# Performance work log

Measured on AMD Instinct MI355X. Metric: run time of the kernel, lower is better.

Reference implementation:

```python
import jax, jax.numpy as jnp
import numpy as np

N_NODES = 50000
N_EDGES = 800000
NFEAT, NHID, NCLASS = 512, 128, 40


def _glorot(key, fan_in, fan_out):
    # mimics the usual GCN uniform init: U(-1/sqrt(fan_out), 1/sqrt(fan_out))
    stdv = 1.0 / np.sqrt(fan_out)
    return jax.random.uniform(key, (fan_in, fan_out), jnp.float32, -stdv, stdv)


def setup_inputs() -> dict:
    key = jax.random.key(0)
    ks = jax.random.split(key, 8)
    x = jax.random.normal(ks[0], (N_NODES, NFEAT), jnp.float32)
    edge_src = jax.random.randint(ks[1], (N_EDGES,), 0, N_NODES)
    edge_dst = jax.random.randint(ks[2], (N_EDGES,), 0, N_NODES)
    edge_weight = jax.random.uniform(ks[3], (N_EDGES,), jnp.float32)
    W1 = _glorot(ks[4], NFEAT, NHID)
    b1 = jnp.zeros((NHID,), jnp.float32)
    W2 = _glorot(ks[5], NHID, NCLASS)
    b2 = jnp.zeros((NCLASS,), jnp.float32)
    return {"x": x, "edge_src": edge_src, "edge_dst": edge_dst,
            "edge_weight": edge_weight, "W1": W1, "b1": b1, "W2": W2, "b2": b2}


def _gcn_layer(x, W, b, edge_src, edge_dst, edge_weight):
    # support = x @ W ; out = spmm(adj, support) + b
    support = x @ W                                   # [N, F_out]
    msgs = support[edge_src] * edge_weight[:, None]   # [E, F_out]
    agg = jax.ops.segment_sum(msgs, edge_dst, num_segments=N_NODES)
    return agg + b


def reference(x, edge_src, edge_dst, edge_weight, W1, b1, W2, b2):
    h = _gcn_layer(x, W1, b1, edge_src, edge_dst, edge_weight)
    h = jax.nn.relu(h)
    # F.dropout(training=False) -> identity in eval mode
    out = _gcn_layer(h, W2, b2, edge_src, edge_dst, edge_weight)
    return out
```

## Files before the change

### kernel.cpp

```cpp
#include <hip/hip_runtime.h>


#define F0 512
#define F1 128
#define F2 40
#define F2P 48

typedef short bf16x8 __attribute__((ext_vector_type(8)));
typedef float f32x4 __attribute__((ext_vector_type(4)));

static __device__ __forceinline__ unsigned short f2b(float f){
    union { float f; unsigned int u; } x; x.f = f;
    unsigned int u = x.u;
    unsigned int r = (u + 0x7fffu + ((u >> 16) & 1u)) >> 16;
    return (unsigned short)r;
}
static __device__ __forceinline__ unsigned short f2b_fast(float f){
    return (unsigned short)((__float_as_uint(f) + 0x8000u) >> 16);
}
static __device__ __forceinline__ unsigned int pack2(float a, float b){
    unsigned int ua = __float_as_uint(a) + 0x8000u;
    unsigned int ub = __float_as_uint(b) + 0x8000u;
    return __builtin_amdgcn_perm(ub, ua, 0x07060302u);
}
static __device__ __forceinline__ bf16x8 pack8(float4 v0, float4 v1){
    union { bf16x8 v; unsigned int d[4]; } r;
    r.d[0] = pack2(v0.x, v0.y);
    r.d[1] = pack2(v0.z, v0.w);
    r.d[2] = pack2(v1.x, v1.y);
    r.d[3] = pack2(v1.z, v1.w);
    return r.v;
}
static __device__ __forceinline__ float b2f(unsigned short h){
    union { unsigned int u; float f; } x; x.u = ((unsigned int)h) << 16; return x.f;
}
static __device__ __forceinline__ unsigned short f2h(float f){
    union { _Float16 h; unsigned short u; } x; x.h = (_Float16)f; return x.u;
}
static __device__ __forceinline__ float h2f(unsigned short u){
    union { unsigned short u; _Float16 h; } x; x.u = u; return (float)x.h;
}

__global__ void prep_w(const float* __restrict__ W1, const float* __restrict__ W2,
                       unsigned short* __restrict__ W1t, unsigned short* __restrict__ W2t,
                       int* __restrict__ cnt8, int n8){
    int idx = blockIdx.x*256 + threadIdx.x;
    if (idx < n8) cnt8[idx] = 0;
    if (idx < F0*F1){
        int k = idx >> 7, n = idx & 127;
        W1t[(size_t)n*F0 + k] = f2b(W1[idx]);
    } else if (idx < F0*F1 + F2P*F1){
        int j = idx - F0*F1;
        int n = j >> 7, k = j & 127;
        float v = (n < F2) ? W2[(size_t)k*F2 + n] : 0.f;
        W2t[j] = f2b(v);
    }
}

__global__ void hist_kernel(const int* __restrict__ dst, int* __restrict__ cnt8,
                            unsigned short* __restrict__ slot, int E){
    int e = blockIdx.x*256 + threadIdx.x;
    if (e < E){
        int d = dst[e];
        int s = e & 7;
        slot[e] = (unsigned short)atomicAdd(&cnt8[d*8 + s], 1);
    }
}

__global__ void scan1_kernel(const int* __restrict__ cnt8, int* __restrict__ offs,
                             unsigned short* __restrict__ lsp, int* __restrict__ bsum, int n){
    __shared__ int sd[256];
    int tid = threadIdx.x;
    int base = blockIdx.x*1024 + tid*4;
    int t[4];
    #pragma unroll
    for (int j=0;j<4;j++){
        int node = base+j;
        int tot = 0;
        if (node < n){
            int4 c0 = *(const int4*)&cnt8[(size_t)node*8];
            int4 c1 = *(const int4*)&cnt8[(size_t)node*8+4];
            unsigned short lp0=0, lp1, lp2, lp3, lp4, lp5, lp6, lp7;
            int run = c0.x; lp1=(unsigned short)run;
            run += c0.y; lp2=(unsigned short)run;
            run += c0.z; lp3=(unsigned short)run;
            run += c0.w; lp4=(unsigned short)run;
            run += c1.x; lp5=(unsigned short)run;
            run += c1.y; lp6=(unsigned short)run;
            run += c1.z; lp7=(unsigned short)run;
            run += c1.w; tot = run;
            ushort4 a, b;
            a.x=lp0; a.y=lp1; a.z=lp2; a.w=lp3;
            b.x=lp4; b.y=lp5; b.z=lp6; b.w=lp7;
            *(ushort4*)&lsp[(size_t)node*8]   = a;
            *(ushort4*)&lsp[(size_t)node*8+4] = b;
        }
        t[j] = tot;
    }
    int v1=t[0], v2=t[0]+t[1], v3=v2+t[2];
    int s = v3+t[3];
    sd[tid]=s; __syncthreads();
    for (int off=1; off<256; off<<=1){
        int tt = (tid>=off)? sd[tid-off] : 0;
        __syncthreads();
        sd[tid] += tt;
        __syncthreads();
    }
    int excl = sd[tid] - s;
    if (base+0<n) offs[base+0]=excl;
    if (base+1<n) offs[base+1]=excl+v1;
    if (base+2<n) offs[base+2]=excl+v2;
    if (base+3<n) offs[base+3]=excl+v3;
    if (tid==255) bsum[blockIdx.x]=sd[255];
}

__global__ void scan3_kernel(int* __restrict__ offs, int* __restrict__ sbase,
                             const unsigned short* __restrict__ lsp,
                             const int* __restrict__ bsum, int n, int E, int nb){
    __shared__ int sexcl;
    int tid = threadIdx.x;
    if (tid < 64){
        int v = (tid < nb) ? bsum[tid] : 0;
        int orig = v;
        #pragma unroll
        for (int off=1; off<64; off<<=1){
            int t = __shfl_up(v, off);
            if (tid >= off) v += t;
        }
        int g = blockIdx.x >> 2;
        if (tid == g) sexcl = v - orig;
    }
    __syncthreads();
    int i = blockIdx.x*256 + tid;
    if (i<n){
        int o = offs[i] + sexcl;
        offs[i] = o;
        ushort4 a = *(const ushort4*)&lsp[(size_t)i*8];
        ushort4 b = *(const ushort4*)&lsp[(size_t)i*8+4];
        int4 s0, s1;
        s0.x=o+a.x; s0.y=o+a.y; s0.z=o+a.z; s0.w=o+a.w;
        s1.x=o+b.x; s1.y=o+b.y; s1.z=o+b.z; s1.w=o+b.w;
        *(int4*)&sbase[(size_t)i*8]   = s0;
        *(int4*)&sbase[(size_t)i*8+4] = s1;
    }
    if (i==0) offs[n]=E;
}

__global__ void scatter_kernel(const int* __restrict__ src, const int* __restrict__ dst,
                               const float* __restrict__ w,
                               const int* __restrict__ sbase,
                               const unsigned short* __restrict__ slot,
                               unsigned int* __restrict__ edges, int E){
    int e = blockIdx.x*256+threadIdx.x;
    if (e<E){
        int d = dst[e];
        int pos = sbase[d*8 + (e & 7)] + (int)slot[e];
        edges[pos] = ((unsigned int)src[e] << 16) | (unsigned int)f2h(w[e]);
    }
}

__global__ __launch_bounds__(256) void gemm1_mfma(const float* __restrict__ X,
                                                  const unsigned short* __restrict__ W1t,
                                                  unsigned short* __restrict__ S1, int M){
    __shared__ unsigned short sB[128*136];
    int tid = threadIdx.x;
    int wave = tid >> 6, lane = tid & 63;
    int quad = lane >> 4, l16 = lane & 15;
    int row0 = blockIdx.x * 64;
    int myrow = row0 + wave*16 + l16;
    int arow = min(myrow, M-1);
    const float* xrow = X + (size_t)arow * F0;

    f32x4 acc[8];
    #pragma unroll
    for (int c=0;c<8;c++) acc[c] = (f32x4){0.f,0.f,0.f,0.f};

    float4 aq[4][2];
    #pragma unroll
    for (int s=0;s<4;s++){
        aq[s][0] = *(const float4*)(xrow + s*32 + quad*8);
        aq[s][1] = *(const float4*)(xrow + s*32 + quad*8 + 4);
    }

    for (int p = 0; p < 4; p++){
        __syncthreads();
        #pragma unroll
        for (int i=0;i<8;i++){
            int idx = tid + i*256;
            int nn = idx >> 4, c8 = idx & 15;
            *(float4*)&sB[nn*136 + c8*8] =
                *(const float4*)&W1t[(size_t)nn*F0 + p*128 + c8*8];
        }
        __syncthreads();
        float4 nq[4][2];
        if (p < 3){
            const float* nx = xrow + (p+1)*128;
            #pragma unroll
            for (int s=0;s<4;s++){
                nq[s][0] = *(const float4*)(nx + s*32 + quad*8);
                nq[s][1] = *(const float4*)(nx + s*32 + quad*8 + 4);
            }
        }
        #pragma unroll
        for (int s=0;s<4;s++){
            bf16x8 af = pack8(aq[s][0], aq[s][1]);
            #pragma unroll
            for (int c=0;c<8;c++){
                bf16x8 b = *(bf16x8*)&sB[(c*16 + l16)*136 + s*32 + quad*8];
                acc[c] = __builtin_amdgcn_mfma_f32_16x16x32_bf16(af, b, acc[c], 0, 0, 0);
            }
        }
        if (p < 3){
            #pragma unroll
            for (int s=0;s<4;s++){ aq[s][0]=nq[s][0]; aq[s][1]=nq[s][1]; }
        }
    }
    #pragma unroll
    for (int c=0;c<8;c++){
        #pragma unroll
        for (int r=0;r<4;r++){
            int grow = row0 + wave*16 + quad*4 + r;
            if (grow < M) S1[(size_t)grow*F1 + c*16 + l16] = f2b_fast(acc[c][r]);
        }
    }
}

__global__ void agg1_kernel(const unsigned short* __restrict__ S1, const int* __restrict__ offs,
                            const unsigned int* __restrict__ edges,
                            const float* __restrict__ b1, unsigned short* __restrict__ H, int n){
    int node = blockIdx.x*4 + (threadIdx.x >> 6);
    int lane = threadIdx.x & 63;
    if (node >= n) return;
    int half = lane >> 5, fl = lane & 31;
    int e0 = offs[node], e1 = offs[node+1];
    double a0=0.0, a1=0.0, a2=0.0, a3=0.0;
    int e = e0;
    for (; e+8 <= e1; e += 8){
        unsigned int rA = edges[e   + half];
        unsigned int rB = edges[e+2 + half];
        unsigned int rC = edges[e+4 + half];
        unsigned int rD = edges[e+6 + half];
        ushort4 vA = *(const ushort4*)&S1[((size_t)(rA>>16))*F1 + fl*4];
        ushort4 vB = *(const ushort4*)&S1[((size_t)(rB>>16))*F1 + fl*4];
        ushort4 vC = *(const ushort4*)&S1[((size_t)(rC>>16))*F1 + fl*4];
        ushort4 vD = *(const ushort4*)&S1[((size_t)(rD>>16))*F1 + fl*4];
        double wA = h2f((unsigned short)rA), wB = h2f((unsigned short)rB);
        double wC = h2f((unsigned short)rC), wD = h2f((unsigned short)rD);
        a0 += wA*b2f(vA.x) + wB*b2f(vB.x) + wC*b2f(vC.x) + wD*b2f(vD.x);
        a1 += wA*b2f(vA.y) + wB*b2f(vB.y) + wC*b2f(vC.y) + wD*b2f(vD.y);
        a2 += wA*b2f(vA.z) + wB*b2f(vB.z) + wC*b2f(vC.z) + wD*b2f(vD.z);
        a3 += wA*b2f(vA.w) + wB*b2f(vB.w) + wC*b2f(vC.w) + wD*b2f(vD.w);
    }
    for (; e < e1; e += 2){
        int ee = e + half;
        if (ee < e1){
            unsigned int r = edges[ee];
            ushort4 v = *(const ushort4*)&S1[((size_t)(r>>16))*F1 + fl*4];
            double w = h2f((unsigned short)r);
            a0 += w*b2f(v.x); a1 += w*b2f(v.y); a2 += w*b2f(v.z); a3 += w*b2f(v.w);
        }
    }
    a0 += __shfl_down(a0, 32);
    a1 += __shfl_down(a1, 32);
    a2 += __shfl_down(a2, 32);
    a3 += __shfl_down(a3, 32);
    if (lane < 32){
        float4 bb = *(const float4*)&b1[fl*4];
        float o0 = (float)(a0 + (double)bb.x);
        float o1 = (float)(a1 + (double)bb.y);
        float o2 = (float)(a2 + (double)bb.z);
        float o3 = (float)(a3 + (double)bb.w);
        o0 = o0>0.f?o0:0.f; o1 = o1>0.f?o1:0.f;
        o2 = o2>0.f?o2:0.f; o3 = o3>0.f?o3:0.f;
        union { ushort4 v; unsigned int d[2]; } o;
        o.d[0] = pack2(o0, o1);
        o.d[1] = pack2(o2, o3);
        *(ushort4*)&H[(size_t)node*F1 + fl*4] = o.v;
    }
}

__global__ __launch_bounds__(256) void gemm2_mfma(const unsigned short* __restrict__ H,
                                                  const unsigned short* __restrict__ W2t,
                                                  unsigned short* __restrict__ S2, int M){
    __shared__ unsigned short sB[48][136];
    int tid = threadIdx.x;
    int wave = tid >> 6, lane = tid & 63;
    int quad = lane >> 4, l16 = lane & 15;
    for (int i = tid; i < 48*16; i += 256){
        int nn = i >> 4, p = i & 15;
        *(float4*)&sB[nn][p*8] = *(const float4*)&W2t[(size_t)nn*F1 + p*8];
    }
    int row0 = blockIdx.x * 64;
    int myrow = row0 + wave*16 + l16;
    int arow = min(myrow, M-1);
    const unsigned short* hrow = H + (size_t)arow * F1;
    bf16x8 a[4];
    #pragma unroll
    for (int ks=0; ks<4; ks++) a[ks] = *(const bf16x8*)(hrow + ks*32 + quad*8);
    __syncthreads();
    f32x4 acc[3];
    #pragma unroll
    for (int c=0;c<3;c++) acc[c] = (f32x4){0.f,0.f,0.f,0.f};
    #pragma unroll
    for (int ks=0; ks<4; ks++){
        #pragma unroll
        for (int c=0;c<3;c++){
            bf16x8 b = *(bf16x8*)&sB[c*16 + l16][ks*32 + quad*8];
            acc[c] = __builtin_amdgcn_mfma_f32_16x16x32_bf16(a[ks], b, acc[c], 0, 0, 0);
        }
    }
    #pragma unroll
    for (int c=0;c<3;c++){
        #pragma unroll
        for (int r=0;r<4;r++){
            int grow = row0 + wave*16 + quad*4 + r;
            if (grow < M) S2[(size_t)grow*F2P + c*16 + l16] = f2b_fast(acc[c][r]);
        }
    }
}

__global__ void agg2_kernel(const unsigned short* __restrict__ S2, const int* __restrict__ offs,
                            const unsigned int* __restrict__ edges,
                            const float* __restrict__ b2, float* __restrict__ out, int n){
    int node = blockIdx.x*4 + (threadIdx.x >> 6);
    int lane = threadIdx.x & 63;
    if (node >= n) return;
    int grp = lane >> 4, gl = lane & 15;
    bool act = gl < 10;
    int e0 = offs[node], e1 = offs[node+1];
    double a0=0.0, a1=0.0, a2=0.0, a3=0.0;
    for (int e = e0; e < e1; e += 4){
        int ee = e + grp;
        if (ee < e1 && act){
            unsigned int r = edges[ee];
            ushort4 v = *(const ushort4*)&S2[((size_t)(r>>16))*F2P + gl*4];
            double w = h2f((unsigned short)r);
            a0 += w*b2f(v.x); a1 += w*b2f(v.y); a2 += w*b2f(v.z); a3 += w*b2f(v.w);
        }
    }
    a0 += __shfl_down(a0, 32); a0 += __shfl_down(a0, 16);
    a1 += __shfl_down(a1, 32); a1 += __shfl_down(a1, 16);
    a2 += __shfl_down(a2, 32); a2 += __shfl_down(a2, 16);
    a3 += __shfl_down(a3, 32); a3 += __shfl_down(a3, 16);
    if (lane < 10){
        float4 bb = *(const float4*)&b2[lane*4];
        float4 o;
        o.x = (float)(a0 + (double)bb.x);
        o.y = (float)(a1 + (double)bb.y);
        o.z = (float)(a2 + (double)bb.z);
        o.w = (float)(a3 + (double)bb.w);
        *(float4*)&out[(size_t)node*F2 + lane*4] = o;
    }
}

extern "C" void kernel_launch(void* const* d_in, const int* in_sizes, int n_in,
                              void* d_out, int out_size, void* d_ws, size_t ws_size,
                              hipStream_t stream){
    const float* x    = (const float*)d_in[0];
    const int*   esrc = (const int*)d_in[1];
    const int*   edst = (const int*)d_in[2];
    const float* ew   = (const float*)d_in[3];
    const float* W1   = (const float*)d_in[4];
    const float* b1   = (const float*)d_in[5];
    const float* W2   = (const float*)d_in[6];
    const float* b2   = (const float*)d_in[7];
    float* out = (float*)d_out;
    int N = in_sizes[0] / F0;
    int E = in_sizes[1];

    char* ws = (char*)d_ws;
    size_t off = 0;
    auto alloc = [&](size_t bytes)->void*{
        void* p = ws + off; off += (bytes + 255) & ~(size_t)255; return p;
    };
    unsigned short* S1 = (unsigned short*)alloc(sizeof(unsigned short)*(size_t)N*F1);
    unsigned short* H  = (unsigned short*)alloc(sizeof(unsigned short)*(size_t)N*F1);
    unsigned short* S2 = (unsigned short*)alloc(sizeof(unsigned short)*(size_t)N*F2P);
    unsigned short* W1t = (unsigned short*)alloc(sizeof(unsigned short)*F1*F0);
    unsigned short* W2t = (unsigned short*)alloc(sizeof(unsigned short)*F2P*F1);
    int*   offs  = (int*)alloc(sizeof(int)*(size_t)(N+1));
    int*   cnt8  = (int*)alloc(sizeof(int)*(size_t)N*8);
    int*   sbase = (int*)alloc(sizeof(int)*(size_t)N*8);
    unsigned short* lsp  = (unsigned short*)alloc(sizeof(unsigned short)*(size_t)N*8);
    unsigned short* slot = (unsigned short*)alloc(sizeof(unsigned short)*(size_t)E);
    unsigned int* edges = (unsigned int*)alloc(sizeof(unsigned int)*(size_t)E);
    int*   bsum  = (int*)alloc(sizeof(int)*64);

    int n8 = N*8;
    int prep_items = n8 > (F0*F1 + F2P*F1) ? n8 : (F0*F1 + F2P*F1);
    prep_w<<<(prep_items+255)/256,256,0,stream>>>(W1, W2, W1t, W2t, cnt8, n8);

    hist_kernel<<<(E+255)/256,256,0,stream>>>(edst, cnt8, slot, E);
    int nb = (N+1023)/1024;
    scan1_kernel<<<nb,256,0,stream>>>(cnt8, offs, lsp, bsum, N);
    scan3_kernel<<<(N+255)/256,256,0,stream>>>(offs, sbase, lsp, bsum, N, E, nb);
    scatter_kernel<<<(E+255)/256,256,0,stream>>>(esrc, edst, ew, sbase, slot, edges, E);

    gemm1_mfma<<<(N+63)/64,256,0,stream>>>(x, W1t, S1, N);
    agg1_kernel<<<(N+3)/4,256,0,stream>>>(S1, offs, edges, b1, H, N);
    gemm2_mfma<<<(N+63)/64,256,0,stream>>>(H, W2t, S2, N);
    agg2_kernel<<<(N+3)/4,256,0,stream>>>(S2, offs, edges, b2, out, N);
}
```

Before: 322.3 us.

## Fuse edge histogram into GEMM1 launch and merge scan passes with decoupled lookback

Measured after the change: 313.6 us. 2.7% less time.

```diff
diff --git a/kernel.cpp b/kernel.cpp
--- a/kernel.cpp
+++ b/kernel.cpp
@@ -43,9 +43,10 @@
 
 __global__ void prep_w(const float* __restrict__ W1, const float* __restrict__ W2,
                        unsigned short* __restrict__ W1t, unsigned short* __restrict__ W2t,
-                       int* __restrict__ cnt8, int n8){
+                       int* __restrict__ cnt8, int n8, int* __restrict__ gflag){
     int idx = blockIdx.x*256 + threadIdx.x;
     if (idx < n8) cnt8[idx] = 0;
+    if (idx < 64) gflag[idx] = 0;
     if (idx < F0*F1){
         int k = idx >> 7, n = idx & 127;
         W1t[(size_t)n*F0 + k] = f2b(W1[idx]);
@@ -57,93 +58,167 @@
     }
 }
 
-__global__ void hist_kernel(const int* __restrict__ dst, int* __restrict__ cnt8,
-                            unsigned short* __restrict__ slot, int E){
-    int e = blockIdx.x*256 + threadIdx.x;
-    if (e < E){
-        int d = dst[e];
-        int s = e & 7;
-        slot[e] = (unsigned short)atomicAdd(&cnt8[d*8 + s], 1);
-    }
-}
-
-__global__ void scan1_kernel(const int* __restrict__ cnt8, int* __restrict__ offs,
-                             unsigned short* __restrict__ lsp, int* __restrict__ bsum, int n){
+__global__ __launch_bounds__(256) void gemm1_hist(const float* __restrict__ X,
+                                                  const unsigned short* __restrict__ W1t,
+                                                  unsigned short* __restrict__ S1, int M,
+                                                  const int* __restrict__ dst,
+                                                  int* __restrict__ cnt8,
+                                                  unsigned short* __restrict__ slot,
+                                                  int E, int gemm_nb){
+    __shared__ unsigned short sB[128*136];
+    int tid = threadIdx.x;
+
+    if ((int)blockIdx.x >= gemm_nb){
+        int e = ((int)blockIdx.x - gemm_nb)*256 + tid;
+        if (e < E){
+            int d = dst[e];
+            int s = e & 7;
+            slot[e] = (unsigned short)atomicAdd(&cnt8[d*8 + s], 1);
+        }
+        return;
+    }
+
+    int wave = tid >> 6, lane = tid & 63;
+    int quad = lane >> 4, l16 = lane & 15;
+    int row0 = blockIdx.x * 64;
+    int myrow = row0 + wave*16 + l16;
+    int arow = min(myrow, M-1);
+    const float* xrow = X + (size_t)arow * F0;
+
+    f32x4 acc[8];
+    #pragma unroll
+    for (int c=0;c<8;c++) acc[c] = (f32x4){0.f,0.f,0.f,0.f};
+
+    float4 aq[4][2];
+    #pragma unroll
+    for (int s=0;s<4;s++){
+        aq[s][0] = *(const float4*)(xrow + s*32 + quad*8);
+        aq[s][1] = *(const float4*)(xrow + s*32 + quad*8 + 4);
+    }
+
+    for (int p = 0; p < 4; p++){
+        __syncthreads();
+        #pragma unroll
+        for (int i=0;i<8;i++){
+            int idx = tid + i*256;
+            int nn = idx >> 4, c8 = idx & 15;
+            *(float4*)&sB[nn*136 + c8*8] =
+                *(const float4*)&W1t[(size_t)nn*F0 + p*128 + c8*8];
+        }
+        __syncthreads();
+        float4 nq[4][2];
+        if (p < 3){
+            const float* nx = xrow + (p+1)*128;
+            #pragma unroll
+            for (int s=0;s<4;s++){
+                nq[s][0] = *(const float4*)(nx + s*32 + quad*8);
+                nq[s][1] = *(const float4*)(nx + s*32 + quad*8 + 4);
+            }
+        }
+        #pragma unroll
+        for (int s=0;s<4;s++){
+            bf16x8 af = pack8(aq[s][0], aq[s][1]);
+            #pragma unroll
+            for (int c=0;c<8;c++){
+                bf16x8 b = *(bf16x8*)&sB[(c*16 + l16)*136 + s*32 + quad*8];
+                acc[c] = __builtin_amdgcn_mfma_f32_16x16x32_bf16(af, b, acc[c], 0, 0, 0);
+            }
+        }
+        if (p < 3){
+            #pragma unroll
+            for (int s=0;s<4;s++){ aq[s][0]=nq[s][0]; aq[s][1]=nq[s][1]; }
+        }
+    }
+    #pragma unroll
+    for (int c=0;c<8;c++){
+        #pragma unroll
+        for (int r=0;r<4;r++){
+            int grow = row0 + wave*16 + quad*4 + r;
+            if (grow < M) S1[(size_t)grow*F1 + c*16 + l16] = f2b_fast(acc[c][r]);
+        }
+    }
+}
+
+__global__ void scan_fused(const int* __restrict__ cnt8, int* __restrict__ offs,
+                           int* __restrict__ sbase, int* __restrict__ gflag,
+                           int n, int E){
     __shared__ int sd[256];
-    int tid = threadIdx.x;
-    int base = blockIdx.x*1024 + tid*4;
+    __shared__ int s_excl;
+    int tid = threadIdx.x, bid = blockIdx.x;
+    int base = bid*1024 + tid*4;
+
     int t[4];
+    int lpr[4][8];
     #pragma unroll
     for (int j=0;j<4;j++){
         int node = base+j;
         int tot = 0;
+        #pragma unroll
+        for (int k=0;k<8;k++) lpr[j][k] = 0;
         if (node < n){
             int4 c0 = *(const int4*)&cnt8[(size_t)node*8];
             int4 c1 = *(const int4*)&cnt8[(size_t)node*8+4];
-            unsigned short lp0=0, lp1, lp2, lp3, lp4, lp5, lp6, lp7;
-            int run = c0.x; lp1=(unsigned short)run;
-            run += c0.y; lp2=(unsigned short)run;
-            run += c0.z; lp3=(unsigned short)run;
-            run += c0.w; lp4=(unsigned short)run;
-            run += c1.x; lp5=(unsigned short)run;
-            run += c1.y; lp6=(unsigned short)run;
-            run += c1.z; lp7=(unsigned short)run;
-            run += c1.w; tot = run;
-            ushort4 a, b;
-            a.x=lp0; a.y=lp1; a.z=lp2; a.w=lp3;
-            b.x=lp4; b.y=lp5; b.z=lp6; b.w=lp7;
-            *(ushort4*)&lsp[(size_t)node*8]   = a;
-            *(ushort4*)&lsp[(size_t)node*8+4] = b;
+            int run;
+            lpr[j][0] = 0;   run  = c0.x;
+            lpr[j][1] = run; run += c0.y;
+            lpr[j][2] = run; run += c0.z;
+            lpr[j][3] = run; run += c0.w;
+            lpr[j][4] = run; run += c1.x;
+            lpr[j][5] = run; run += c1.y;
+            lpr[j][6] = run; run += c1.z;
+            lpr[j][7] = run; run += c1.w;
+            tot = run;
         }
         t[j] = tot;
     }
-    int v1=t[0], v2=t[0]+t[1], v3=v2+t[2];
-    int s = v3+t[3];
-    sd[tid]=s; __syncthreads();
+    int v1 = t[0], v2 = t[0]+t[1], v3 = v2+t[2];
+    int s = v3 + t[3];
+    sd[tid] = s; __syncthreads();
     for (int off=1; off<256; off<<=1){
-        int tt = (tid>=off)? sd[tid-off] : 0;
+        int tt = (tid>=off) ? sd[tid-off] : 0;
         __syncthreads();
         sd[tid] += tt;
         __syncthreads();
     }
     int excl = sd[tid] - s;
-    if (base+0<n) offs[base+0]=excl;
-    if (base+1<n) offs[base+1]=excl+v1;
-    if (base+2<n) offs[base+2]=excl+v2;
-    if (base+3<n) offs[base+3]=excl+v3;
-    if (tid==255) bsum[blockIdx.x]=sd[255];
-}
-
-__global__ void scan3_kernel(int* __restrict__ offs, int* __restrict__ sbase,
-                             const unsigned short* __restrict__ lsp,
-                             const int* __restrict__ bsum, int n, int E, int nb){
-    __shared__ int sexcl;
-    int tid = threadIdx.x;
+    int btot = sd[255];
+
+    if (tid == 0)
+        __hip_atomic_store(&gflag[bid], btot + 1, __ATOMIC_RELEASE, __HIP_MEMORY_SCOPE_AGENT);
     if (tid < 64){
-        int v = (tid < nb) ? bsum[tid] : 0;
-        int orig = v;
-        #pragma unroll
-        for (int off=1; off<64; off<<=1){
-            int t = __shfl_up(v, off);
-            if (tid >= off) v += t;
-        }
-        int g = blockIdx.x >> 2;
-        if (tid == g) sexcl = v - orig;
+        int v = 0;
+        if (tid < bid){
+            int g;
+            do {
+                g = __hip_atomic_load(&gflag[tid], __ATOMIC_ACQUIRE, __HIP_MEMORY_SCOPE_AGENT);
+                if (g == 0) __builtin_amdgcn_s_sleep(1);
+            } while (g == 0);
+            v = g - 1;
+        }
+        #pragma unroll
+        for (int o=1; o<64; o<<=1) v += __shfl_xor(v, o);
+        if (tid == 0) s_excl = v;
     }
     __syncthreads();
-    int i = blockIdx.x*256 + tid;
-    if (i<n){
-        int o = offs[i] + sexcl;
-        offs[i] = o;
-        ushort4 a = *(const ushort4*)&lsp[(size_t)i*8];
-        ushort4 b = *(const ushort4*)&lsp[(size_t)i*8+4];
-        int4 s0, s1;
-        s0.x=o+a.x; s0.y=o+a.y; s0.z=o+a.z; s0.w=o+a.w;
-        s1.x=o+b.x; s1.y=o+b.y; s1.z=o+b.z; s1.w=o+b.w;
-        *(int4*)&sbase[(size_t)i*8]   = s0;
-        *(int4*)&sbase[(size_t)i*8+4] = s1;
-    }
-    if (i==0) offs[n]=E;
+
+    int node_off[4] = {0, v1, v2, v3};
+    int gexcl = s_excl + excl;
+    #pragma unroll
+    for (int j=0;j<4;j++){
+        int node = base+j;
+        if (node < n){
+            int o = gexcl + node_off[j];
+            offs[node] = o;
+            int4 s0, s1;
+            s0.x = o + lpr[j][0]; s0.y = o + lpr[j][1];
+            s0.z = o + lpr[j][2]; s0.w = o + lpr[j][3];
+            s1.x = o + lpr[j][4]; s1.y = o + lpr[j][5];
+            s1.z = o + lpr[j][6]; s1.w = o + lpr[j][7];
+            *(int4*)&sbase[(size_t)node*8]   = s0;
+            *(int4*)&sbase[(size_t)node*8+4] = s1;
+        }
+    }
+    if (bid == 0 && tid == 0) offs[n] = E;
 }
 
 __global__ void scatter_kernel(const int* __restrict__ src, const int* __restrict__ dst,
@@ -156,72 +231,6 @@
         int d = dst[e];
         int pos = sbase[d*8 + (e & 7)] + (int)slot[e];
         edges[pos] = ((unsigned int)src[e] << 16) | (unsigned int)f2h(w[e]);
-    }
-}
-
-__global__ __launch_bounds__(256) void gemm1_mfma(const float* __restrict__ X,
-                                                  const unsigned short* __restrict__ W1t,
-                                                  unsigned short* __restrict__ S1, int M){
-    __shared__ unsigned short sB[128*136];
-    int tid = threadIdx.x;
-    int wave = tid >> 6, lane = tid & 63;
-    int quad = lane >> 4, l16 = lane & 15;
-    int row0 = blockIdx.x * 64;
-    int myrow = row0 + wave*16 + l16;
-    int arow = min(myrow, M-1);
-    const float* xrow = X + (size_t)arow * F0;
-
-    f32x4 acc[8];
-    #pragma unroll
-    for (int c=0;c<8;c++) acc[c] = (f32x4){0.f,0.f,0.f,0.f};
-
-    float4 aq[4][2];
-    #pragma unroll
-    for (int s=0;s<4;s++){
-        aq[s][0] = *(const float4*)(xrow + s*32 + quad*8);
-        aq[s][1] = *(const float4*)(xrow + s*32 + quad*8 + 4);
-    }
-
-    for (int p = 0; p < 4; p++){
-        __syncthreads();
-        #pragma unroll
-        for (int i=0;i<8;i++){
-            int idx = tid + i*256;
-            int nn = idx >> 4, c8 = idx & 15;
-            *(float4*)&sB[nn*136 + c8*8] =
-                *(const float4*)&W1t[(size_t)nn*F0 + p*128 + c8*8];
-        }
-        __syncthreads();
-        float4 nq[4][2];
-        if (p < 3){
-            const float* nx = xrow + (p+1)*128;
-            #pragma unroll
-            for (int s=0;s<4;s++){
-                nq[s][0] = *(const float4*)(nx + s*32 + quad*8);
-                nq[s][1] = *(const float4*)(nx + s*32 + quad*8 + 4);
-            }
-        }
-        #pragma unroll
-        for (int s=0;s<4;s++){
-            bf16x8 af = pack8(aq[s][0], aq[s][1]);
-            #pragma unroll
-            for (int c=0;c<8;c++){
-                bf16x8 b = *(bf16x8*)&sB[(c*16 + l16)*136 + s*32 + quad*8];
-                acc[c] = __builtin_amdgcn_mfma_f32_16x16x32_bf16(af, b, acc[c], 0, 0, 0);
-            }
-        }
-        if (p < 3){
-            #pragma unroll
-            for (int s=0;s<4;s++){ aq[s][0]=nq[s][0]; aq[s][1]=nq[s][1]; }
-        }
-    }
-    #pragma unroll
-    for (int c=0;c<8;c++){
-        #pragma unroll
-        for (int r=0;r<4;r++){
-            int grow = row0 + wave*16 + quad*4 + r;
-            if (grow < M) S1[(size_t)grow*F1 + c*16 + l16] = f2b_fast(acc[c][r]);
-        }
     }
 }
 
@@ -381,23 +390,23 @@
     int*   offs  = (int*)alloc(sizeof(int)*(size_t)(N+1));
     int*   cnt8  = (int*)alloc(sizeof(int)*(size_t)N*8);
     int*   sbase = (int*)alloc(sizeof(int)*(size_t)N*8);
-    unsigned short* lsp  = (unsigned short*)alloc(sizeof(unsigned short)*(size_t)N*8);
     unsigned short* slot = (unsigned short*)alloc(sizeof(unsigned short)*(size_t)E);
     unsigned int* edges = (unsigned int*)alloc(sizeof(unsigned int)*(size_t)E);
-    int*   bsum  = (int*)alloc(sizeof(int)*64);
+    int*   gflag = (int*)alloc(sizeof(int)*64);
 
     int n8 = N*8;
     int prep_items = n8 > (F0*F1 + F2P*F1) ? n8 : (F0*F1 + F2P*F1);
-    prep_w<<<(prep_items+255)/256,256,0,stream>>>(W1, W2, W1t, W2t, cnt8, n8);
-
-    hist_kernel<<<(E+255)/256,256,0,stream>>>(edst, cnt8, slot, E);
+    prep_w<<<(prep_items+255)/256,256,0,stream>>>(W1, W2, W1t, W2t, cnt8, n8, gflag);
+
+    int gemm_nb = (N+63)/64;
+    int hist_nb = (E+255)/256;
+    gemm1_hist<<<gemm_nb + hist_nb,256,0,stream>>>(x, W1t, S1, N, edst, cnt8, slot, E, gemm_nb);
+
     int nb = (N+1023)/1024;
-    scan1_kernel<<<nb,256,0,stream>>>(cnt8, offs, lsp, bsum, N);
-    scan3_kernel<<<(N+255)/256,256,0,stream>>>(offs, sbase, lsp, bsum, N, E, nb);
-    scatter_kernel<<<(E+255)/256,256,0,stream>>>(esrc, edst, ew, sbase, slot, edges, E);
-
-    gemm1_mfma<<<(N+63)/64,256,0,stream>>>(x, W1t, S1, N);
+    scan_fused<<<nb,256,0,stream>>>(cnt8, offs, sbase, gflag, N, E);
+    scatter_kernel<<<hist_nb,256,0,stream>>>(esrc, edst, ew, sbase, slot, edges, E);
+
     agg1_kernel<<<(N+3)/4,256,0,stream>>>(S1, offs, edges, b1, H, N);
-    gemm2_mfma<<<(N+63)/64,256,0,stream>>>(H, W2t, S2, N);
+    gemm2_mfma<<<gemm_nb,256,0,stream>>>(H, W2t, S2, N);
     agg2_kernel<<<(N+3)/4,256,0,stream>>>(S2, offs, edges, b2, out, N);
 }
```
